# Kernel tuning notes

Hardware: AMD Instinct MI355X
Metric: run time of the kernel (lower is better)

## Reference

```python
import jax, jax.numpy as jnp
import numpy as np


def fwht(x):
    """Fast Walsh-Hadamard transform along last axis (n must be a power of 2).
    Loop runs log2(n) times (fixed, ~12 iters) -- fully vectorized butterflies."""
    n = x.shape[-1]
    prefix = x.shape[:-1]
    x = x.reshape(-1, n)
    h = 1
    while h < n:
        x = x.reshape(-1, n // (2 * h), 2, h)
        a, b = x[:, :, 0, :], x[:, :, 1, :]
        x = jnp.stack([a + b, a - b], axis=2).reshape(-1, n)
        h *= 2
    return x.reshape(prefix + (n,))


def setup_inputs() -> dict:
    key = jax.random.key(0)
    ks = jax.random.split(key, 8)
    Bz, S, N, M = 4, 2048, 4096, 4096   # batch, seq, in_features, out_features
    CODESZ, CB_SIZE, RANK = 8, 256, 64
    inp = {}
    inp["input"] = jax.random.normal(ks[0], (Bz, S, N), dtype=jnp.float32)
    inp["Qidxs"] = jax.random.randint(ks[1], (M, N // CODESZ), 0, CB_SIZE, dtype=jnp.int32)
    inp["codebook_vals"] = jax.random.normal(ks[2], (CB_SIZE, CODESZ), dtype=jnp.float32)
    # SU/SV are random sign vectors in QuIP#
    inp["SU"] = jnp.sign(jax.random.normal(ks[3], (N,), dtype=jnp.float32))
    inp["SV"] = jnp.sign(jax.random.normal(ks[4], (M,), dtype=jnp.float32))
    inp["Wscale"] = jnp.ones((), dtype=jnp.float32)
    inp["A"] = jax.random.normal(ks[5], (M, RANK), dtype=jnp.float32) * 0.01
    inp["B"] = jax.random.normal(ks[6], (RANK, N), dtype=jnp.float32) * 0.01
    return inp


def reference(input, Qidxs, codebook_vals, SU, SV, Wscale, A, B):
    n = SU.shape[0]   # in_features
    m = SV.shape[0]   # out_features
    lead = input.shape[:-1]
    x = input.reshape(-1, n).astype(jnp.float32)          # [T, n]
    # input rotation: x <- H^T (x * SU) / sqrt(n)   (matmul_hadUt, K=1 case)
    x = fwht(x * SU) * (1.0 / jnp.sqrt(jnp.float32(n)))
    # low-rank correction branch (rank > 0)
    Bx = x @ B.T                                          # [T, rank]
    # dequantize: codebook lookup [m, n/codesz, codesz] -> [m, n]
    W = codebook_vals[Qidxs].reshape(m, n)
    z = (x @ W.T) * Wscale                                # [T, m]
    z = z + Bx @ A.T
    # output rotation: z <- SV * (H z) / sqrt(m)
    z = fwht(z) * (1.0 / jnp.sqrt(jnp.float32(m))) * SV
    return z.reshape(lead + (m,))
```

## Files before the change

kernel.cpp:

```cpp
#include <hip/hip_runtime.h>
#include <hip/hip_bf16.h>


typedef __attribute__((ext_vector_type(8))) short short8;
typedef __attribute__((ext_vector_type(4))) float f32x4;

#define T_ROWS 8192
#define NDIM   4096
#define MDIM   4096
#define NT     (NDIM / 64)

__device__ __forceinline__ void gld_lds16(const void* g, void* lds_uniform) {
    __builtin_amdgcn_global_load_lds(
        (const __attribute__((address_space(1))) unsigned int*)(unsigned long long)(uintptr_t)g,
        (__attribute__((address_space(3))) unsigned int*)(unsigned int)(uintptr_t)lds_uniform,
        16, 0, 0);
}

__device__ __forceinline__ void bfly(float& a, float& b) {
    float s = a + b, d = a - b; a = s; b = d;
}

__device__ __forceinline__ void fwht16(float* v) {
#pragma unroll
    for (int h = 1; h <= 8; h <<= 1)
#pragma unroll
        for (int j = 0; j < 16; ++j)
            if (!(j & h)) bfly(v[j], v[j | h]);
}

__global__ __launch_bounds__(256) void fwht_in_kernel(
        const float* __restrict__ in, const float* __restrict__ SU,
        __hip_bfloat16* __restrict__ xout) {
    __shared__ float sh[4352];
    const int t = threadIdx.x;
    const size_t r = blockIdx.x;
    float v[16];
    {
        const float4* s4 = (const float4*)(in + (r << 12) + t * 16);
        const float4* u4 = (const float4*)(SU + t * 16);
#pragma unroll
        for (int q = 0; q < 4; ++q) {
            float4 a = s4[q], u = u4[q];
            v[4 * q + 0] = a.x * u.x; v[4 * q + 1] = a.y * u.y;
            v[4 * q + 2] = a.z * u.z; v[4 * q + 3] = a.w * u.w;
        }
    }
    fwht16(v);
#pragma unroll
    for (int j = 0; j < 16; ++j) sh[17 * t + j] = v[j];
    __syncthreads();
    const int baseB = (t & 15) + 272 * (t >> 4);
#pragma unroll
    for (int j = 0; j < 16; ++j) v[j] = sh[baseB + 17 * j];
    fwht16(v);
#pragma unroll
    for (int j = 0; j < 16; ++j) sh[baseB + 17 * j] = v[j];
    __syncthreads();
    const int baseC = t + (t >> 4);
#pragma unroll
    for (int j = 0; j < 16; ++j) v[j] = sh[baseC + 272 * j];
    fwht16(v);
    __hip_bfloat16* dst = xout + (r << 12);
#pragma unroll
    for (int j = 0; j < 16; ++j)
        dst[(j << 8) + t] = __float2bfloat16(v[j] * 0.015625f);
}

__global__ __launch_bounds__(256) void fwht_out_kernel(
        float* __restrict__ z, const float* __restrict__ SV) {
    __shared__ float sh[4352];
    const int t = threadIdx.x;
    const size_t r = blockIdx.x;
    float* row = z + (r << 12);
    float v[16];
    {
        const float4* s4 = (const float4*)(row + t * 16);
#pragma unroll
        for (int q = 0; q < 4; ++q) {
            float4 a = s4[q];
            v[4 * q + 0] = a.x; v[4 * q + 1] = a.y;
            v[4 * q + 2] = a.z; v[4 * q + 3] = a.w;
        }
    }
    fwht16(v);
#pragma unroll
    for (int j = 0; j < 16; ++j) sh[17 * t + j] = v[j];
    __syncthreads();
    const int baseB = (t & 15) + 272 * (t >> 4);
#pragma unroll
    for (int j = 0; j < 16; ++j) v[j] = sh[baseB + 17 * j];
    fwht16(v);
#pragma unroll
    for (int j = 0; j < 16; ++j) sh[baseB + 17 * j] = v[j];
    __syncthreads();
    const int baseC = t + (t >> 4);
#pragma unroll
    for (int j = 0; j < 16; ++j) v[j] = sh[baseC + 272 * j];
    fwht16(v);
#pragma unroll
    for (int j = 0; j < 16; ++j)
        row[(j << 8) + t] = v[j] * 0.015625f * SV[(j << 8) + t];
}

__global__ __launch_bounds__(256) void dequant_kernel(
        const int* __restrict__ Qidxs, const float* __restrict__ cb,
        const float* __restrict__ Wscale, const float* __restrict__ A,
        const float* __restrict__ B, __hip_bfloat16* __restrict__ Weff) {
    __shared__ float At[64][68];
    __shared__ float Bs[64][68];
    __shared__ float cbs[2048];
    const int t = threadIdx.x;
    const int i0 = blockIdx.y * 64, j0 = blockIdx.x * 64;

    {
        const float* ga = A + (size_t)i0 * 64;
        const int r = t >> 2, kb = (t & 3) * 16;
#pragma unroll
        for (int j = 0; j < 16; ++j) At[kb + j][r] = ga[t * 16 + j];
        const int k = t >> 2, c0 = (t & 3) * 16;
        const float* gb = B + (size_t)k * NDIM + j0 + c0;
#pragma unroll
        for (int j = 0; j < 16; ++j) Bs[k][c0 + j] = gb[j];
#pragma unroll
        for (int j = 0; j < 8; ++j) cbs[t * 8 + j] = cb[t * 8 + j];
    }
    __syncthreads();

    const int ty = t >> 4, tx = t & 15;
    float acc[4][4];
#pragma unroll
    for (int a = 0; a < 4; ++a)
#pragma unroll
        for (int b = 0; b < 4; ++b) acc[a][b] = 0.f;

#pragma unroll 8
    for (int k = 0; k < 64; ++k) {
        const float4 av = *(const float4*)&At[k][ty * 4];
        const float4 bv = *(const float4*)&Bs[k][tx * 4];
        const float aa[4] = {av.x, av.y, av.z, av.w};
        const float bb[4] = {bv.x, bv.y, bv.z, bv.w};
#pragma unroll
        for (int ii = 0; ii < 4; ++ii)
#pragma unroll
            for (int jj = 0; jj < 4; ++jj) acc[ii][jj] += aa[ii] * bb[jj];
    }

    const float wsc = Wscale[0];
#pragma unroll
    for (int ii = 0; ii < 4; ++ii) {
        const int i = i0 + ty * 4 + ii;
        const int* qrow = Qidxs + (size_t)i * (NDIM / 8);
        union { __hip_bfloat16 h[4]; unsigned long long u; } pk;
#pragma unroll
        for (int jj = 0; jj < 4; ++jj) {
            const int j = j0 + tx * 4 + jj;
            const int idx = qrow[j >> 3];
            const float val = cbs[idx * 8 + (j & 7)] * wsc + acc[ii][jj];
            pk.h[jj] = __float2bfloat16(val);
        }
        *(unsigned long long*)&Weff[(size_t)i * NDIM + j0 + tx * 4] = pk.u;
    }
}

__global__ __launch_bounds__(512, 2) void gemm256_kernel(
        const __hip_bfloat16* __restrict__ X, const __hip_bfloat16* __restrict__ W,
        float* __restrict__ Z) {
    __shared__ short smem[65536];

    const int b = blockIdx.x;
    const int swz = (b & 7) * 64 + (b >> 3);
    const int bm = swz >> 4, bn = swz & 15;

    const int tid = threadIdx.x;
    const int lane = tid & 63, wid = tid >> 6;
    const int wm = wid >> 2, wn = wid & 3;
    const int lr = lane & 15, lk = lane >> 4;
    const int swb = (lr & 7) << 4;
    const int c0 = (((lk << 4)) ^ swb) >> 1;
    const int c1 = ((64 | (lk << 4)) ^ swb) >> 1;
    const int wbase = wid << 9;

    const int grow = tid >> 3;
    const int scol = (((tid & 7) ^ (grow & 7)) << 3);
    const __hip_bfloat16* gA = X + (size_t)(bm * 256 + grow) * NDIM + scol;
    const __hip_bfloat16* gB = W + (size_t)(bn * 256 + grow) * NDIM + scol;

#define STA2(OFS, H, Q, BUF) gld_lds16(gA + (size_t)(((H) * 128 + (Q) * 64) * NDIM) + (OFS), \
        &smem[(BUF) * 32768 + (H) * 8192 + (Q) * 4096 + wbase])
#define STB2(OFS, H, Q, BUF) gld_lds16(gB + (size_t)(((H) * 128 + (Q) * 64) * NDIM) + (OFS), \
        &smem[(BUF) * 32768 + 16384 + (H) * 8192 + (Q) * 4096 + wbase])
#define STAGE_A(OFS, BUF) do { STA2(OFS,0,0,BUF); STA2(OFS,0,1,BUF); \
                               STA2(OFS,1,0,BUF); STA2(OFS,1,1,BUF); } while (0)
#define STAGE_B(OFS, BUF) do { STB2(OFS,0,0,BUF); STB2(OFS,0,1,BUF); \
                               STB2(OFS,1,0,BUF); STB2(OFS,1,1,BUF); } while (0)

#define RDA(D0, D1, D2, D3, M0, AB) do { \
    D0 = *(const short8*)((AB) + ((M0) * 16 + lr) * 64 + c0); \
    D1 = *(const short8*)((AB) + ((M0) * 16 + lr) * 64 + c1); \
    D2 = *(const short8*)((AB) + ((M0) * 16 + 16 + lr) * 64 + c0); \
    D3 = *(const short8*)((AB) + ((M0) * 16 + 16 + lr) * 64 + c1); \
} while (0)

#define RDB(BARR, BUF) do { \
    const short* bB_ = smem + (BUF) * 32768 + 16384 + (wn * 64 + lr) * 64; \
    _Pragma("unroll") \
    for (int n = 0; n < 4; ++n) { \
        BARR[2 * n]     = *(const short8*)(bB_ + n * 1024 + c0); \
        BARR[2 * n + 1] = *(const short8*)(bB_ + n * 1024 + c1); \
    } \
} while (0)

#define MFMA2(A0, A1, E0, E1, M0, BF) do { \
    __builtin_amdgcn_s_setprio(1); \
    _Pragma("unroll") \
    for (int n = 0; n < 4; ++n) \
        acc[M0][n] = __builtin_amdgcn_mfma_f32_16x16x32_bf16(A0, BF[2 * n], acc[M0][n], 0, 0, 0); \
    _Pragma("unroll") \
    for (int n = 0; n < 4; ++n) \
        acc[(M0) + 1][n] = __builtin_amdgcn_mfma_f32_16x16x32_bf16(E0, BF[2 * n], acc[(M0) + 1][n], 0, 0, 0); \
    _Pragma("unroll") \
    for (int n = 0; n < 4; ++n) \
        acc[M0][n] = __builtin_amdgcn_mfma_f32_16x16x32_bf16(A1, BF[2 * n + 1], acc[M0][n], 0, 0, 0); \
    _Pragma("unroll") \
    for (int n = 0; n < 4; ++n) \
        acc[(M0) + 1][n] = __builtin_amdgcn_mfma_f32_16x16x32_bf16(E1, BF[2 * n + 1], acc[(M0) + 1][n], 0, 0, 0); \
    __builtin_amdgcn_s_setprio(0); \
} while (0)

#define TILE(CUR, BF, BN, DO_STA, DO_STB, DO_PF, VMMID, LAST) do { \
    const short* aBase = smem + (CUR) * 32768 + wm * 8192; \
    if (DO_STA) STAGE_A(64, 1 - (CUR)); \
    if (DO_STB) STAGE_B(128, (CUR)); \
    RDA(t0, t1, t2, t3, 2, aBase); \
    MFMA2(p0, p1, p2, p3, 0, BF); \
    RDA(p0, p1, p2, p3, 4, aBase); \
    MFMA2(t0, t1, t2, t3, 2, BF); \
    RDA(t0, t1, t2, t3, 6, aBase); \
    MFMA2(p0, p1, p2, p3, 4, BF); \
    if (DO_PF) { \
        asm volatile("s_waitcnt vmcnt(" #VMMID ")" ::: "memory"); \
        __builtin_amdgcn_s_barrier(); \
        RDB(BN, 1 - (CUR)); \
        RDA(p0, p1, p2, p3, 0, smem + (1 - (CUR)) * 32768 + wm * 8192); \
        __builtin_amdgcn_sched_barrier(0); \
    } \
    MFMA2(t0, t1, t2, t3, 6, BF); \
    if (!(LAST)) { \
        asm volatile("s_waitcnt lgkmcnt(0)" ::: "memory"); \
        __builtin_amdgcn_s_barrier(); \
    } \
    gA += 64; gB += 64; \
} while (0)

    f32x4 acc[8][4];
#pragma unroll
    for (int m = 0; m < 8; ++m)
#pragma unroll
        for (int n = 0; n < 4; ++n) acc[m][n] = 0.f;

    short8 B0r[8], B1r[8];
    short8 p0, p1, p2, p3, t0, t1, t2, t3;

    STAGE_A(0, 0);
    STAGE_B(0, 0);
    STAGE_B(64, 1);
    asm volatile("s_waitcnt vmcnt(4)" ::: "memory");
    __builtin_amdgcn_s_barrier();
    RDB(B0r, 0);
    RDA(p0, p1, p2, p3, 0, smem + wm * 8192);
    asm volatile("s_waitcnt lgkmcnt(0)" ::: "memory");
    __builtin_amdgcn_s_barrier();

    for (int i = 0; i < 31; ++i) {
        TILE(0, B0r, B1r, 1, 1, 1, 4, 0);
        TILE(1, B1r, B0r, 1, 1, 1, 4, 0);
    }
    TILE(0, B0r, B1r, 1, 0, 1, 0, 0);
    TILE(1, B1r, B0r, 0, 0, 0, 0, 1);

    const size_t r0 = (size_t)bm * 256 + wm * 128 + (lk << 2);
    const size_t cb0 = (size_t)bn * 256 + wn * 64 + lr;
#pragma unroll
    for (int m = 0; m < 8; ++m)
#pragma unroll
        for (int n = 0; n < 4; ++n) {
            const size_t col = cb0 + n * 16;
#pragma unroll
            for (int j = 0; j < 4; ++j)
                Z[(r0 + m * 16 + j) * MDIM + col] = acc[m][n][j];
        }
}

extern "C" void kernel_launch(void* const* d_in, const int* in_sizes, int n_in,
                              void* d_out, int out_size, void* d_ws, size_t ws_size,
                              hipStream_t stream) {
    const float* input  = (const float*)d_in[0];
    const int*   Qidxs  = (const int*)d_in[1];
    const float* cbvals = (const float*)d_in[2];
    const float* SU     = (const float*)d_in[3];
    const float* SV     = (const float*)d_in[4];
    const float* Wscale = (const float*)d_in[5];
    const float* A      = (const float*)d_in[6];
    const float* B      = (const float*)d_in[7];
    float* out = (float*)d_out;

    __hip_bfloat16* xbf = (__hip_bfloat16*)d_ws;
    __hip_bfloat16* wbf = (__hip_bfloat16*)((char*)d_ws + (size_t)T_ROWS * NDIM * 2);

    fwht_in_kernel<<<T_ROWS, 256, 0, stream>>>(input, SU, xbf);
    dequant_kernel<<<dim3(MDIM / 64, MDIM / 64), 256, 0, stream>>>(
        Qidxs, cbvals, Wscale, A, B, wbf);
    gemm256_kernel<<<(T_ROWS / 256) * (MDIM / 256), 512, 0, stream>>>(xbf, wbf, out);
    fwht_out_kernel<<<T_ROWS, 256, 0, stream>>>(out, SV);
}
```

Baseline: 379.5 us.

## Simplify GEMM tile pipeline: drop mid-tile barrier, setprio, cross-tile A prefetch

Restructures the per-tile schedule of the main bf16 GEMM loop. The mid-tile vmcnt wait plus barrier and the cross-tile A-fragment prefetch are removed, as are the s_setprio hints around MFMA groups. The tile now reads all A fragments from the current buffer and prefetches the next B fragments late in the tile. To stay correct it waits for all outstanding global loads (vmcnt(0)) at the end-of-tile barrier. This drops one barrier per tile but serialises global-load completion at tile boundaries and gives up the MFMA priority hints, which may weaken load/compute overlap.

```diff
diff --git a/kernel.cpp b/kernel.cpp
--- a/kernel.cpp
+++ b/kernel.cpp
@@ -212,7 +212,6 @@
 } while (0)
 
 #define MFMA2(A0, A1, E0, E1, M0, BF) do { \
-    __builtin_amdgcn_s_setprio(1); \
     _Pragma("unroll") \
     for (int n = 0; n < 4; ++n) \
         acc[M0][n] = __builtin_amdgcn_mfma_f32_16x16x32_bf16(A0, BF[2 * n], acc[M0][n], 0, 0, 0); \
@@ -225,29 +224,24 @@
     _Pragma("unroll") \
     for (int n = 0; n < 4; ++n) \
         acc[(M0) + 1][n] = __builtin_amdgcn_mfma_f32_16x16x32_bf16(E1, BF[2 * n + 1], acc[(M0) + 1][n], 0, 0, 0); \
-    __builtin_amdgcn_s_setprio(0); \
 } while (0)
 
-#define TILE(CUR, BF, BN, DO_STA, DO_STB, DO_PF, VMMID, LAST) do { \
+#define TILE(CUR, BF, BN, DO_STA, DO_STB, DO_BN, LAST) do { \
     const short* aBase = smem + (CUR) * 32768 + wm * 8192; \
     if (DO_STA) STAGE_A(64, 1 - (CUR)); \
     if (DO_STB) STAGE_B(128, (CUR)); \
-    RDA(t0, t1, t2, t3, 2, aBase); \
-    MFMA2(p0, p1, p2, p3, 0, BF); \
-    RDA(p0, p1, p2, p3, 4, aBase); \
-    MFMA2(t0, t1, t2, t3, 2, BF); \
-    RDA(t0, t1, t2, t3, 6, aBase); \
-    MFMA2(p0, p1, p2, p3, 4, BF); \
-    if (DO_PF) { \
-        asm volatile("s_waitcnt vmcnt(" #VMMID ")" ::: "memory"); \
-        __builtin_amdgcn_s_barrier(); \
-        RDB(BN, 1 - (CUR)); \
-        RDA(p0, p1, p2, p3, 0, smem + (1 - (CUR)) * 32768 + wm * 8192); \
-        __builtin_amdgcn_sched_barrier(0); \
-    } \
-    MFMA2(t0, t1, t2, t3, 6, BF); \
+    RDA(xa0, xa1, xb0, xb1, 0, aBase); \
+    RDA(ya0, ya1, yb0, yb1, 2, aBase); \
+    MFMA2(xa0, xa1, xb0, xb1, 0, BF); \
+    RDA(xa0, xa1, xb0, xb1, 4, aBase); \
+    MFMA2(ya0, ya1, yb0, yb1, 2, BF); \
+    RDA(ya0, ya1, yb0, yb1, 6, aBase); \
+    if (DO_BN) RDB(BN, 1 - (CUR)); \
+    MFMA2(xa0, xa1, xb0, xb1, 4, BF); \
+    MFMA2(ya0, ya1, yb0, yb1, 6, BF); \
     if (!(LAST)) { \
         asm volatile("s_waitcnt lgkmcnt(0)" ::: "memory"); \
+        asm volatile("s_waitcnt vmcnt(0)" ::: "memory"); \
         __builtin_amdgcn_s_barrier(); \
     } \
     gA += 64; gB += 64; \
@@ -260,24 +254,23 @@
         for (int n = 0; n < 4; ++n) acc[m][n] = 0.f;
 
     short8 B0r[8], B1r[8];
-    short8 p0, p1, p2, p3, t0, t1, t2, t3;
+    short8 xa0, xa1, xb0, xb1, ya0, ya1, yb0, yb1;
 
     STAGE_A(0, 0);
     STAGE_B(0, 0);
     STAGE_B(64, 1);
-    asm volatile("s_waitcnt vmcnt(4)" ::: "memory");
+    asm volatile("s_waitcnt vmcnt(0)" ::: "memory");
     __builtin_amdgcn_s_barrier();
     RDB(B0r, 0);
-    RDA(p0, p1, p2, p3, 0, smem + wm * 8192);
     asm volatile("s_waitcnt lgkmcnt(0)" ::: "memory");
     __builtin_amdgcn_s_barrier();
 
     for (int i = 0; i < 31; ++i) {
-        TILE(0, B0r, B1r, 1, 1, 1, 4, 0);
-        TILE(1, B1r, B0r, 1, 1, 1, 4, 0);
-    }
-    TILE(0, B0r, B1r, 1, 0, 1, 0, 0);
-    TILE(1, B1r, B0r, 0, 0, 0, 0, 1);
+        TILE(0, B0r, B1r, 1, 1, 1, 0);
+        TILE(1, B1r, B0r, 1, 1, 1, 0);
+    }
+    TILE(0, B0r, B1r, 1, 0, 1, 0);
+    TILE(1, B1r, B0r, 0, 0, 0, 1);
 
     const size_t r0 = (size_t)bm * 256 + wm * 128 + (lk << 2);
     const size_t cb0 = (size_t)bn * 256 + wn * 64 + lr;
```

Measured after the change: 356.9 us. -6.0%, faster.
